# Optimization experiments

Hardware: AMD Instinct MI355X
Metric: run time of the kernel (lower is better)

Reference implementation:

```python
import jax, jax.numpy as jnp
from jax import lax
import numpy as np

B = 2; Hs = 48; Ws = 48
DIM = 768; NH = 6; NP = 4; DH = DIM // NH; HID = int(DIM * 0.25)
LIN = Hs * Ws                    # feat tokens (single deform level)
LQ = 21 * (Hs * Ws) // 4         # query tokens: (2H*2W)+(H*W)+(H/2*W/2)


def _ln(x, g, b, eps=1e-6):
    m = jnp.mean(x, -1, keepdims=True)
    v = jnp.mean((x - m) ** 2, -1, keepdims=True)
    return (x - m) * lax.rsqrt(v + eps) * g + b


def _bilinear_sample(value, loc, Hf, Wf):
    """value: [B,NH,Hf*Wf,DH]; loc: [B,Lq,NH,NP,2] normalized to [0,1].
    Matches F.grid_sample(align_corners=False, padding_mode='zeros')."""
    Bq, nH = value.shape[0], value.shape[1]
    Lq = loc.shape[1]
    x = loc[..., 0] * Wf - 0.5
    y = loc[..., 1] * Hf - 0.5
    x0 = jnp.floor(x); y0 = jnp.floor(y)
    wx1 = x - x0; wy1 = y - y0
    x0i = x0.astype(jnp.int32); y0i = y0.astype(jnp.int32)

    def tr(a):  # [B,Lq,NH,NP] -> [B,NH,Lq*NP]
        return jnp.transpose(a, (0, 2, 1, 3)).reshape(Bq, nH, Lq * NP)

    def gather(yi, xi):
        valid = ((xi >= 0) & (xi < Wf) & (yi >= 0) & (yi < Hf)).astype(value.dtype)
        idx = jnp.clip(yi, 0, Hf - 1) * Wf + jnp.clip(xi, 0, Wf - 1)
        g = jnp.take_along_axis(value, tr(idx)[..., None], axis=2)  # [B,NH,Lq*NP,DH]
        return g * tr(valid)[..., None]

    out = (gather(y0i, x0i) * tr((1 - wy1) * (1 - wx1))[..., None]
         + gather(y0i, x0i + 1) * tr((1 - wy1) * wx1)[..., None]
         + gather(y0i + 1, x0i) * tr(wy1 * (1 - wx1))[..., None]
         + gather(y0i + 1, x0i + 1) * tr(wy1 * wx1)[..., None])
    return out.reshape(Bq, nH, Lq, NP, DH)


def _dwconv(x_tokens, w, b, h, w_):
    Bq, n_tok, C = x_tokens.shape
    img = jnp.transpose(x_tokens, (0, 2, 1)).reshape(Bq, C, h, w_)
    y = lax.conv_general_dilated(img, w, (1, 1), 'SAME',
                                 dimension_numbers=('NCHW', 'OIHW', 'NCHW'),
                                 feature_group_count=C) + b[None, :, None, None]
    return jnp.transpose(y.reshape(Bq, C, h * w_), (0, 2, 1))


def _forward(query, reference_points, feat, qn_g, qn_b, fn_g, fn_b, vW, vb,
             soW, sob, awW, awb, opW, opb, mn_g, mn_b,
             fc1W, fc1b, dwW, dwb, fc2W, fc2b, H, W):
    Bq, Lq, C = query.shape
    q = _ln(query, qn_g, qn_b)
    v = _ln(feat, fn_g, fn_b) @ vW + vb                             # [B,Lin,C]
    value = jnp.transpose(v.reshape(Bq, -1, NH, DH), (0, 2, 1, 3))  # [B,NH,Lin,DH]
    offs = (q @ soW + sob).reshape(Bq, Lq, NH, NP, 2)
    attw = jax.nn.softmax((q @ awW + awb).reshape(Bq, Lq, NH, NP), axis=-1)
    norm = jnp.asarray([W, H], dtype=q.dtype)                       # (x,y) normalizer
    loc = reference_points.reshape(Bq, Lq, 1, 1, 2) + offs / norm   # [B,Lq,NH,NP,2]
    samp = _bilinear_sample(value, loc, H, W)                       # [B,NH,Lq,NP,DH]
    aw = jnp.transpose(attw, (0, 2, 1, 3))[..., None]               # [B,NH,Lq,NP,1]
    out = jnp.sum(samp * aw, axis=3)                                # [B,NH,Lq,DH]
    out = jnp.transpose(out, (0, 2, 1, 3)).reshape(Bq, Lq, C) @ opW + opb
    x = query + out                                                 # residual
    # multi-scale conv MLP
    h = _ln(x, mn_g, mn_b) @ fc1W + fc1b                            # [B,Lq,HID]
    n = Lq // 21
    h = jnp.concatenate([
        _dwconv(h[:, :16 * n], dwW, dwb, 2 * H, 2 * W),
        _dwconv(h[:, 16 * n:20 * n], dwW, dwb, H, W),
        _dwconv(h[:, 20 * n:], dwW, dwb, H // 2, W // 2)], axis=1)
    h = jax.nn.gelu(h, approximate=False)
    h = h @ fc2W + fc2b
    return x + h


def setup_inputs():
    key = jax.random.key(0)
    ks = jax.random.split(key, 16)
    s = 0.02
    return dict(
        query=jax.random.normal(ks[0], (B, LQ, DIM), jnp.float32),
        reference_points=jax.random.uniform(ks[1], (B, LQ, 1, 2), jnp.float32),
        feat=jax.random.normal(ks[2], (B, LIN, DIM), jnp.float32),
        spatial_shapes=jnp.array([[Hs, Ws]], jnp.int32),
        level_start_index=jnp.array([0], jnp.int32),
        H=Hs, W=Ws,
        qn_g=jnp.ones((DIM,)), qn_b=jnp.zeros((DIM,)),
        fn_g=jnp.ones((DIM,)), fn_b=jnp.zeros((DIM,)),
        mn_g=jnp.ones((DIM,)), mn_b=jnp.zeros((DIM,)),
        vW=s * jax.random.normal(ks[3], (DIM, DIM)), vb=jnp.zeros((DIM,)),
        soW=s * jax.random.normal(ks[4], (DIM, NH * NP * 2)),
        sob=0.5 * jax.random.normal(ks[5], (NH * NP * 2,)),
        awW=s * jax.random.normal(ks[6], (DIM, NH * NP)), awb=jnp.zeros((NH * NP,)),
        opW=s * jax.random.normal(ks[7], (DIM, DIM)), opb=jnp.zeros((DIM,)),
        fc1W=s * jax.random.normal(ks[8], (DIM, HID)), fc1b=jnp.zeros((HID,)),
        dwW=s * jax.random.normal(ks[9], (HID, 1, 3, 3)), dwb=jnp.zeros((HID,)),
        fc2W=s * jax.random.normal(ks[10], (HID, DIM)), fc2b=jnp.zeros((DIM,)),
    )


def reference(query, reference_points, feat, spatial_shapes, level_start_index, H, W,
              qn_g, qn_b, fn_g, fn_b, mn_g, mn_b, vW, vb, soW, sob, awW, awb,
              opW, opb, fc1W, fc1b, dwW, dwb, fc2W, fc2b):
    del spatial_shapes, level_start_index  # single level; H,W are static ints
    return _forward(query, reference_points, feat, qn_g, qn_b, fn_g, fn_b, vW, vb,
                    soW, sob, awW, awb, opW, opb, mn_g, mn_b,
                    fc1W, fc1b, dwW, dwb, fc2W, fc2b, H, W)
```

## Files before the change

### kernel.cpp

```cpp
#include <hip/hip_runtime.h>

#define NB    2
#define LQT   12096
#define LINT  2304
#define DIMC  768
#define NHD   6
#define NPT   4
#define DHD   128
#define HIDC  192
#define HH    48
#define WW    48

typedef __attribute__((ext_vector_type(8))) short bf16x8;
typedef __attribute__((ext_vector_type(4))) float f32x4;
typedef __attribute__((ext_vector_type(8))) unsigned short u16x8;

__device__ __forceinline__ unsigned short f2bf(float f) {
  unsigned int u = __builtin_bit_cast(unsigned int, f);
  u += 0x7FFFu + ((u >> 16) & 1u);
  return (unsigned short)(u >> 16);
}

__device__ __forceinline__ void gload16(const unsigned short* g, unsigned short* l) {
  __builtin_amdgcn_global_load_lds(
      (const __attribute__((address_space(1))) unsigned int*)g,
      (__attribute__((address_space(3))) unsigned int*)l, 16, 0, 0);
}

__global__ __launch_bounds__(256) void pack_wt(const float* __restrict__ src,
                                               unsigned short* __restrict__ dst,
                                               int K, int N, int rows) {
  size_t i = (size_t)blockIdx.x * 256 + threadIdx.x;
  if (i >= (size_t)rows * K) return;
  int n = (int)(i / K), k = (int)(i % K);
  float v = (n < N) ? src[(size_t)k * N + n] : 0.f;
  dst[i] = f2bf(v);
}

__global__ __launch_bounds__(256) void pack_soaw(const float* __restrict__ soW,
                                                 const float* __restrict__ awW,
                                                 const float* __restrict__ sob,
                                                 const float* __restrict__ awb,
                                                 unsigned short* __restrict__ dst,
                                                 float* __restrict__ bdst) {
  size_t i = (size_t)blockIdx.x * 256 + threadIdx.x;
  if (i < 128) bdst[i] = (i < 48) ? sob[i] : (i < 72 ? awb[i - 48] : 0.f);
  if (i >= (size_t)128 * DIMC) return;
  int n = (int)(i / DIMC), k = (int)(i % DIMC);
  float v = (n < 48) ? soW[(size_t)k * 48 + n]
                     : (n < 72 ? awW[(size_t)k * 24 + (n - 48)] : 0.f);
  dst[i] = f2bf(v);
}

__global__ __launch_bounds__(256) void ln_to_bf16(const float* __restrict__ in,
                                                  const float* __restrict__ gamma,
                                                  const float* __restrict__ beta,
                                                  unsigned short* __restrict__ out) {
  const int row = blockIdx.x;
  const int t = threadIdx.x;
  const float* x = in + (size_t)row * DIMC;
  float v0 = x[t], v1 = x[t + 256], v2 = x[t + 512];
  float s = v0 + v1 + v2;
  float s2 = v0 * v0 + v1 * v1 + v2 * v2;
#pragma unroll
  for (int o = 32; o > 0; o >>= 1) {
    s += __shfl_down(s, o);
    s2 += __shfl_down(s2, o);
  }
  __shared__ float red[8];
  const int wave = t >> 6, lane = t & 63;
  if (lane == 0) { red[wave] = s; red[wave + 4] = s2; }
  __syncthreads();
  float S = red[0] + red[1] + red[2] + red[3];
  float S2 = red[4] + red[5] + red[6] + red[7];
  float mean = S * (1.0f / DIMC);
  float var = S2 * (1.0f / DIMC) - mean * mean;
  float inv = rsqrtf(var + 1e-6f);
  unsigned short* o0 = out + (size_t)row * DIMC;
  o0[t]       = f2bf((v0 - mean) * inv * gamma[t]       + beta[t]);
  o0[t + 256] = f2bf((v1 - mean) * inv * gamma[t + 256] + beta[t + 256]);
  o0[t + 512] = f2bf((v2 - mean) * inv * gamma[t + 512] + beta[t + 512]);
}

template <bool HAS_ADD>
__global__ __launch_bounds__(256) void gemm_bt(const unsigned short* __restrict__ A,
                                               const unsigned short* __restrict__ Bt,
                                               const float* __restrict__ bias,
                                               const float* __restrict__ add,
                                               float* __restrict__ out,
                                               int M, int N, int K, int nn) {
  __shared__ unsigned short As[3][128 * 32];
  __shared__ unsigned short Bs[3][128 * 32];
  const int t = threadIdx.x;
  const int wave = t >> 6, lane = t & 63;

  const int nwg = gridDim.x;
  const int qq = nwg >> 3, rr = nwg & 7;
  const int xcd = blockIdx.x & 7, pos = blockIdx.x >> 3;
  const int swz = ((xcd < rr) ? xcd * (qq + 1) : rr * (qq + 1) + (xcd - rr) * qq) + pos;
  const int m0 = (swz / nn) * 128;
  const int n0 = (swz % nn) * 128;

  const int wm = (wave >> 1) * 64, wn = (wave & 1) * 64;
  const int lr = lane & 15;
  const int lg = lane >> 4;

  const int srow = wave * 16 + (lane >> 2);
  const int sslot = lane & 3;

  auto stage = [&](int buf, int k0) {
#pragma unroll
    for (int i = 0; i < 2; ++i) {
      const int row = srow + i * 64;
      const int ca = sslot ^ ((row >> 1) & 3);
      gload16(A  + (size_t)(m0 + row) * K + k0 + ca * 8, &As[buf][(wave * 16 + i * 64) * 32]);
      gload16(Bt + (size_t)(n0 + row) * K + k0 + ca * 8, &Bs[buf][(wave * 16 + i * 64) * 32]);
    }
  };

  f32x4 acc[4][4] = {};
  const int NT = K >> 5;

  stage(0, 0);
  if (NT > 1) stage(1, 32);
  if (NT > 2) stage(2, 64);

  int buf = 0;
  for (int kt = 0; kt < NT; ++kt) {
    if (kt < NT - 2)       asm volatile("s_waitcnt vmcnt(8)" ::: "memory");
    else if (kt == NT - 2) asm volatile("s_waitcnt vmcnt(4)" ::: "memory");
    else                   asm volatile("s_waitcnt vmcnt(0)" ::: "memory");
    __builtin_amdgcn_s_barrier();
    __builtin_amdgcn_sched_barrier(0);

    bf16x8 af[4], bg[4];
#pragma unroll
    for (int i = 0; i < 4; ++i) {
      int row = wm + i * 16 + lr;
      int slot = lg ^ ((row >> 1) & 3);
      af[i] = *(const bf16x8*)(&As[buf][row * 32 + slot * 8]);
      row = wn + i * 16 + lr;
      slot = lg ^ ((row >> 1) & 3);
      bg[i] = *(const bf16x8*)(&Bs[buf][row * 32 + slot * 8]);
    }
    asm volatile("s_waitcnt lgkmcnt(0)" ::: "memory");
    __builtin_amdgcn_sched_barrier(0);
    __builtin_amdgcn_s_barrier();

    if (kt + 3 < NT) stage(buf, (kt + 3) * 32);

#pragma unroll
    for (int i = 0; i < 4; ++i)
#pragma unroll
      for (int j = 0; j < 4; ++j)
        acc[i][j] = __builtin_amdgcn_mfma_f32_16x16x32_bf16(af[i], bg[j], acc[i][j], 0, 0, 0);

    buf = (buf == 2) ? 0 : buf + 1;
  }

  const int orow = lg * 4;
#pragma unroll
  for (int i = 0; i < 4; ++i) {
#pragma unroll
    for (int j = 0; j < 4; ++j) {
      const int n = n0 + wn + j * 16 + lr;
      if (n < N) {
#pragma unroll
        for (int r = 0; r < 4; ++r) {
          const int m = m0 + wm + i * 16 + orow + r;
          float v = acc[i][j][r] + bias[n];
          if (HAS_ADD) v += add[(size_t)m * N + n];
          out[(size_t)m * N + n] = v;
        }
      }
    }
  }
}

__global__ __launch_bounds__(192) void deform_attn(const float* __restrict__ soaw,
                                                   const float* __restrict__ rp,
                                                   const float* __restrict__ value,
                                                   unsigned short* __restrict__ attn) {
  const int row = blockIdx.x;
  const int b = row / LQT;
  const int t = threadIdx.x;
  const int h = t >> 5;
  const int l = t & 31;
  const float* sa = soaw + (size_t)row * 128;
  const float bx = rp[(size_t)row * 2 + 0] * (float)WW - 0.5f;
  const float by = rp[(size_t)row * 2 + 1] * (float)HH - 0.5f;

  float lg0 = sa[48 + h * 4 + 0], lg1 = sa[48 + h * 4 + 1];
  float lg2 = sa[48 + h * 4 + 2], lg3 = sa[48 + h * 4 + 3];
  float mx = fmaxf(fmaxf(lg0, lg1), fmaxf(lg2, lg3));
  float e0 = expf(lg0 - mx), e1 = expf(lg1 - mx), e2 = expf(lg2 - mx), e3 = expf(lg3 - mx);
  float inv = 1.0f / (e0 + e1 + e2 + e3);
  float awp[4] = {e0 * inv, e1 * inv, e2 * inv, e3 * inv};

  const float* vb = value + (size_t)b * LINT * DIMC + h * DHD + l * 4;
  float ax = 0.f, ay = 0.f, az = 0.f, aw = 0.f;
#pragma unroll
  for (int p = 0; p < 4; ++p) {
    float fx = bx + sa[h * 8 + p * 2 + 0];
    float fy = by + sa[h * 8 + p * 2 + 1];
    float x0f = floorf(fx), y0f = floorf(fy);
    float wx = fx - x0f, wy = fy - y0f;
    int x0 = (int)x0f, y0 = (int)y0f;
#pragma unroll
    for (int dy = 0; dy < 2; ++dy) {
#pragma unroll
      for (int dx = 0; dx < 2; ++dx) {
        int xi = x0 + dx, yi = y0 + dy;
        float w = (dy ? wy : 1.f - wy) * (dx ? wx : 1.f - wx) * awp[p];
        if (xi < 0 || xi >= WW || yi < 0 || yi >= HH) w = 0.f;
        int xc = min(max(xi, 0), WW - 1), yc = min(max(yi, 0), HH - 1);
        const float4 g = *(const float4*)(vb + (size_t)(yc * WW + xc) * DIMC);
        ax += w * g.x; ay += w * g.y; az += w * g.z; aw += w * g.w;
      }
    }
  }
  unsigned short* op = attn + (size_t)row * DIMC + h * DHD + l * 4;
  ushort4 ov;
  ov.x = f2bf(ax); ov.y = f2bf(ay); ov.z = f2bf(az); ov.w = f2bf(aw);
  *(ushort4*)op = ov;
}

__global__ __launch_bounds__(192) void dwconv_gelu(const float* __restrict__ h1,
                                                   const float* __restrict__ dwW,
                                                   const float* __restrict__ dwb,
                                                   unsigned short* __restrict__ out) {
  const int blk = blockIdx.x;
  const int b = blk / LQT;
  const int q = blk % LQT;
  int base, Wi, Hi;
  if (q < 9216)       { base = 0;     Wi = 96; Hi = 96; }
  else if (q < 11520) { base = 9216;  Wi = 48; Hi = 48; }
  else                { base = 11520; Wi = 24; Hi = 24; }
  const int loc = q - base;
  const int y = loc / Wi, x = loc % Wi;
  const int c = threadIdx.x;
  const float* src = h1 + ((size_t)b * LQT + base) * HIDC + c;
  float acc = dwb[c];
#pragma unroll
  for (int dy = -1; dy <= 1; ++dy) {
    int yy = y + dy;
    if (yy < 0 || yy >= Hi) continue;
#pragma unroll
    for (int dx = -1; dx <= 1; ++dx) {
      int xx = x + dx;
      if (xx < 0 || xx >= Wi) continue;
      acc += dwW[c * 9 + (dy + 1) * 3 + (dx + 1)] * src[(size_t)(yy * Wi + xx) * HIDC];
    }
  }
  float g = 0.5f * acc * (1.0f + erff(acc * 0.70710678118654752f));
  out[(size_t)blk * HIDC + c] = f2bf(g);
}

extern "C" void kernel_launch(void* const* d_in, const int* in_sizes, int n_in,
                              void* d_out, int out_size, void* d_ws, size_t ws_size,
                              hipStream_t stream) {
  const float* query = (const float*)d_in[0];
  const float* rp    = (const float*)d_in[1];
  const float* feat  = (const float*)d_in[2];
  const float* qn_g  = (const float*)d_in[7];
  const float* qn_b  = (const float*)d_in[8];
  const float* fn_g  = (const float*)d_in[9];
  const float* fn_b  = (const float*)d_in[10];
  const float* mn_g  = (const float*)d_in[11];
  const float* mn_b  = (const float*)d_in[12];
  const float* vW    = (const float*)d_in[13];
  const float* vb    = (const float*)d_in[14];
  const float* soW   = (const float*)d_in[15];
  const float* sob   = (const float*)d_in[16];
  const float* awW   = (const float*)d_in[17];
  const float* awb   = (const float*)d_in[18];
  const float* opW   = (const float*)d_in[19];
  const float* opb   = (const float*)d_in[20];
  const float* fc1W  = (const float*)d_in[21];
  const float* fc1b  = (const float*)d_in[22];
  const float* dwW   = (const float*)d_in[23];
  const float* dwb   = (const float*)d_in[24];
  const float* fc2W  = (const float*)d_in[25];
  const float* fc2b  = (const float*)d_in[26];
  float* out = (float*)d_out;
  (void)in_sizes; (void)n_in; (void)out_size; (void)ws_size;

  char* ws = (char*)d_ws;
  size_t off = 0;
  auto alloc = [&](size_t bytes) -> void* {
    off = (off + 255) & ~(size_t)255;
    void* p = ws + off;
    off += bytes;
    return p;
  };

  const int MQ = NB * LQT;
  const int MF = NB * LINT;

  unsigned short* vWt    = (unsigned short*)alloc((size_t)768 * 768 * 2);
  unsigned short* opWt   = (unsigned short*)alloc((size_t)768 * 768 * 2);
  unsigned short* soawWt = (unsigned short*)alloc((size_t)128 * 768 * 2);
  unsigned short* fc1Wt  = (unsigned short*)alloc((size_t)256 * 768 * 2);
  unsigned short* fc2Wt  = (unsigned short*)alloc((size_t)768 * 192 * 2);
  float*          soawb  = (float*)alloc(128 * 4);
  unsigned short* f_ln   = (unsigned short*)alloc((size_t)MF * DIMC * 2);
  unsigned short* q_ln   = (unsigned short*)alloc((size_t)MQ * DIMC * 2);
  float*          value  = (float*)alloc((size_t)MF * DIMC * 4);
  float*          soaw   = (float*)alloc((size_t)MQ * 128 * 4);
  unsigned short* attnb  = (unsigned short*)alloc((size_t)MQ * DIMC * 2);
  float*          xbuf   = (float*)alloc((size_t)MQ * DIMC * 4);

  float* h1 = (float*)attnb;
  unsigned short* coutb = (unsigned short*)soaw;
  unsigned short* lnx = q_ln;

  pack_wt<<<dim3((768 * 768 + 255) / 256), dim3(256), 0, stream>>>(vW, vWt, 768, 768, 768);
  pack_wt<<<dim3((768 * 768 + 255) / 256), dim3(256), 0, stream>>>(opW, opWt, 768, 768, 768);
  pack_wt<<<dim3((256 * 768 + 255) / 256), dim3(256), 0, stream>>>(fc1W, fc1Wt, 768, 192, 256);
  pack_wt<<<dim3((768 * 192 + 255) / 256), dim3(256), 0, stream>>>(fc2W, fc2Wt, 192, 768, 768);
  pack_soaw<<<dim3((128 * 768 + 255) / 256), dim3(256), 0, stream>>>(soW, awW, sob, awb, soawWt, soawb);

  ln_to_bf16<<<dim3(MF), dim3(256), 0, stream>>>(feat, fn_g, fn_b, f_ln);
  ln_to_bf16<<<dim3(MQ), dim3(256), 0, stream>>>(query, qn_g, qn_b, q_ln);

  gemm_bt<false><<<dim3((MF / 128) * 6), dim3(256), 0, stream>>>(f_ln, vWt, vb, nullptr, value, MF, 768, 768, 6);

  gemm_bt<false><<<dim3(MQ / 128), dim3(256), 0, stream>>>(q_ln, soawWt, soawb, nullptr, soaw, MQ, 128, 768, 1);

  deform_attn<<<dim3(MQ), dim3(192), 0, stream>>>(soaw, rp, value, attnb);

  gemm_bt<true><<<dim3((MQ / 128) * 6), dim3(256), 0, stream>>>(attnb, opWt, opb, query, xbuf, MQ, 768, 768, 6);

  ln_to_bf16<<<dim3(MQ), dim3(256), 0, stream>>>(xbuf, mn_g, mn_b, lnx);

  gemm_bt<false><<<dim3((MQ / 128) * 2), dim3(256), 0, stream>>>(lnx, fc1Wt, fc1b, nullptr, h1, MQ, 192, 768, 2);

  dwconv_gelu<<<dim3(MQ), dim3(192), 0, stream>>>(h1, dwW, dwb, coutb);

  gemm_bt<true><<<dim3((MQ / 128) * 6), dim3(256), 0, stream>>>(coutb, fc2Wt, fc2b, xbuf, out, MQ, 768, 192, 6);
}
```

Before: 337.3 us.

## Templatize GEMM tile shapes per layer and store residual intermediate in bf16

The GEMM kernel is now templated on per-wave tile counts, so each layer gets its own block shape. The value and soaw GEMMs use 64x128 tiles, the out-proj uses 256x128 tiles over a padded M, and fc1 uses 128x64 tiles so the padded fc1 weight is no longer needed. The residual buffer xbuf is stored as bf16 and the following LN and fc2 read it as bf16, which halves that traffic. The cost is lower residual precision and reliance on padded attn rows, which are only partly written.

```diff
diff --git a/kernel.cpp b/kernel.cpp
--- a/kernel.cpp
+++ b/kernel.cpp
@@ -13,18 +13,30 @@
 
 typedef __attribute__((ext_vector_type(8))) short bf16x8;
 typedef __attribute__((ext_vector_type(4))) float f32x4;
-typedef __attribute__((ext_vector_type(8))) unsigned short u16x8;
 
 __device__ __forceinline__ unsigned short f2bf(float f) {
   unsigned int u = __builtin_bit_cast(unsigned int, f);
   u += 0x7FFFu + ((u >> 16) & 1u);
   return (unsigned short)(u >> 16);
 }
+__device__ __forceinline__ float bf2f(unsigned short h) {
+  unsigned int u = ((unsigned int)h) << 16;
+  return __builtin_bit_cast(float, u);
+}
 
 __device__ __forceinline__ void gload16(const unsigned short* g, unsigned short* l) {
   __builtin_amdgcn_global_load_lds(
       (const __attribute__((address_space(1))) unsigned int*)g,
       (__attribute__((address_space(3))) unsigned int*)l, 16, 0, 0);
+}
+
+template <int N> __device__ __forceinline__ void wait_vm() {
+  if constexpr (N == 0)       asm volatile("s_waitcnt vmcnt(0)" ::: "memory");
+  else if constexpr (N == 3)  asm volatile("s_waitcnt vmcnt(3)" ::: "memory");
+  else if constexpr (N == 4)  asm volatile("s_waitcnt vmcnt(4)" ::: "memory");
+  else if constexpr (N == 6)  asm volatile("s_waitcnt vmcnt(6)" ::: "memory");
+  else if constexpr (N == 8)  asm volatile("s_waitcnt vmcnt(8)" ::: "memory");
+  else if constexpr (N == 12) asm volatile("s_waitcnt vmcnt(12)" ::: "memory");
 }
 
 __global__ __launch_bounds__(256) void pack_wt(const float* __restrict__ src,
@@ -52,14 +64,21 @@
   dst[i] = f2bf(v);
 }
 
-__global__ __launch_bounds__(256) void ln_to_bf16(const float* __restrict__ in,
+template <bool IN_BF16>
+__global__ __launch_bounds__(256) void ln_to_bf16(const void* __restrict__ in_,
                                                   const float* __restrict__ gamma,
                                                   const float* __restrict__ beta,
                                                   unsigned short* __restrict__ out) {
   const int row = blockIdx.x;
   const int t = threadIdx.x;
-  const float* x = in + (size_t)row * DIMC;
-  float v0 = x[t], v1 = x[t + 256], v2 = x[t + 512];
+  float v0, v1, v2;
+  if (IN_BF16) {
+    const unsigned short* x = (const unsigned short*)in_ + (size_t)row * DIMC;
+    v0 = bf2f(x[t]); v1 = bf2f(x[t + 256]); v2 = bf2f(x[t + 512]);
+  } else {
+    const float* x = (const float*)in_ + (size_t)row * DIMC;
+    v0 = x[t]; v1 = x[t + 256]; v2 = x[t + 512];
+  }
   float s = v0 + v1 + v2;
   float s2 = v0 * v0 + v1 * v1 + v2 * v2;
 #pragma unroll
@@ -82,15 +101,19 @@
   o0[t + 512] = f2bf((v2 - mean) * inv * gamma[t + 512] + beta[t + 512]);
 }
 
-template <bool HAS_ADD>
+template <int WM, int WN, bool HAS_ADD, bool ADD_BF16, bool OUT_BF16>
 __global__ __launch_bounds__(256) void gemm_bt(const unsigned short* __restrict__ A,
                                                const unsigned short* __restrict__ Bt,
                                                const float* __restrict__ bias,
-                                               const float* __restrict__ add,
-                                               float* __restrict__ out,
+                                               const void* __restrict__ add_,
+                                               void* __restrict__ out_,
                                                int M, int N, int K, int nn) {
-  __shared__ unsigned short As[3][128 * 32];
-  __shared__ unsigned short Bs[3][128 * 32];
+  constexpr int BM = 2 * WM * 16;
+  constexpr int BN = 2 * WN * 16;
+  constexpr int LPS = (BM + BN) / 64;
+  constexpr int CA = BM * 4;
+  __shared__ unsigned short As[3][BM * 32];
+  __shared__ unsigned short Bs[3][BN * 32];
   const int t = threadIdx.x;
   const int wave = t >> 6, lane = t & 63;
 
@@ -98,50 +121,56 @@
   const int qq = nwg >> 3, rr = nwg & 7;
   const int xcd = blockIdx.x & 7, pos = blockIdx.x >> 3;
   const int swz = ((xcd < rr) ? xcd * (qq + 1) : rr * (qq + 1) + (xcd - rr) * qq) + pos;
-  const int m0 = (swz / nn) * 128;
-  const int n0 = (swz % nn) * 128;
-
-  const int wm = (wave >> 1) * 64, wn = (wave & 1) * 64;
+  const int m0 = (swz / nn) * BM;
+  const int n0 = (swz % nn) * BN;
+
+  const int wm = (wave >> 1) * (WM * 16), wn = (wave & 1) * (WN * 16);
   const int lr = lane & 15;
   const int lg = lane >> 4;
 
-  const int srow = wave * 16 + (lane >> 2);
-  const int sslot = lane & 3;
-
   auto stage = [&](int buf, int k0) {
 #pragma unroll
-    for (int i = 0; i < 2; ++i) {
-      const int row = srow + i * 64;
-      const int ca = sslot ^ ((row >> 1) & 3);
-      gload16(A  + (size_t)(m0 + row) * K + k0 + ca * 8, &As[buf][(wave * 16 + i * 64) * 32]);
-      gload16(Bt + (size_t)(n0 + row) * K + k0 + ca * 8, &Bs[buf][(wave * 16 + i * 64) * 32]);
+    for (int i = 0; i < LPS; ++i) {
+      const int c = t + i * 256;
+      if (c < CA) {
+        const int row = c >> 2, slot = c & 3;
+        const int ca = slot ^ ((row >> 1) & 3);
+        gload16(A + (size_t)(m0 + row) * K + k0 + ca * 8, &As[buf][c * 8]);
+      } else {
+        const int c2 = c - CA, row = c2 >> 2, slot = c2 & 3;
+        const int ca = slot ^ ((row >> 1) & 3);
+        gload16(Bt + (size_t)(n0 + row) * K + k0 + ca * 8, &Bs[buf][c2 * 8]);
+      }
     }
   };
 
-  f32x4 acc[4][4] = {};
+  f32x4 acc[WM][WN] = {};
   const int NT = K >> 5;
 
   stage(0, 0);
-  if (NT > 1) stage(1, 32);
-  if (NT > 2) stage(2, 64);
+  stage(1, 32);
+  stage(2, 64);
 
   int buf = 0;
   for (int kt = 0; kt < NT; ++kt) {
-    if (kt < NT - 2)       asm volatile("s_waitcnt vmcnt(8)" ::: "memory");
-    else if (kt == NT - 2) asm volatile("s_waitcnt vmcnt(4)" ::: "memory");
-    else                   asm volatile("s_waitcnt vmcnt(0)" ::: "memory");
+    if (kt < NT - 2)       wait_vm<2 * LPS>();
+    else if (kt == NT - 2) wait_vm<LPS>();
+    else                   wait_vm<0>();
     __builtin_amdgcn_s_barrier();
     __builtin_amdgcn_sched_barrier(0);
 
-    bf16x8 af[4], bg[4];
-#pragma unroll
-    for (int i = 0; i < 4; ++i) {
-      int row = wm + i * 16 + lr;
-      int slot = lg ^ ((row >> 1) & 3);
+    bf16x8 af[WM], bg[WN];
+#pragma unroll
+    for (int i = 0; i < WM; ++i) {
+      const int row = wm + i * 16 + lr;
+      const int slot = lg ^ ((row >> 1) & 3);
       af[i] = *(const bf16x8*)(&As[buf][row * 32 + slot * 8]);
-      row = wn + i * 16 + lr;
-      slot = lg ^ ((row >> 1) & 3);
-      bg[i] = *(const bf16x8*)(&Bs[buf][row * 32 + slot * 8]);
+    }
+#pragma unroll
+    for (int j = 0; j < WN; ++j) {
+      const int row = wn + j * 16 + lr;
+      const int slot = lg ^ ((row >> 1) & 3);
+      bg[j] = *(const bf16x8*)(&Bs[buf][row * 32 + slot * 8]);
     }
     asm volatile("s_waitcnt lgkmcnt(0)" ::: "memory");
     __builtin_amdgcn_sched_barrier(0);
@@ -150,27 +179,34 @@
     if (kt + 3 < NT) stage(buf, (kt + 3) * 32);
 
 #pragma unroll
-    for (int i = 0; i < 4; ++i)
-#pragma unroll
-      for (int j = 0; j < 4; ++j)
+    for (int i = 0; i < WM; ++i)
+#pragma unroll
+      for (int j = 0; j < WN; ++j)
         acc[i][j] = __builtin_amdgcn_mfma_f32_16x16x32_bf16(af[i], bg[j], acc[i][j], 0, 0, 0);
 
     buf = (buf == 2) ? 0 : buf + 1;
   }
 
   const int orow = lg * 4;
-#pragma unroll
-  for (int i = 0; i < 4; ++i) {
-#pragma unroll
-    for (int j = 0; j < 4; ++j) {
+  const float* addf = (const float*)add_;
+  const unsigned short* addb = (const unsigned short*)add_;
+  float* outf = (float*)out_;
+  unsigned short* outb = (unsigned short*)out_;
+#pragma unroll
+  for (int i = 0; i < WM; ++i) {
+#pragma unroll
+    for (int j = 0; j < WN; ++j) {
       const int n = n0 + wn + j * 16 + lr;
       if (n < N) {
 #pragma unroll
         for (int r = 0; r < 4; ++r) {
           const int m = m0 + wm + i * 16 + orow + r;
-          float v = acc[i][j][r] + bias[n];
-          if (HAS_ADD) v += add[(size_t)m * N + n];
-          out[(size_t)m * N + n] = v;
+          if (m < M) {
+            float v = acc[i][j][r] + bias[n];
+            if (HAS_ADD) v += ADD_BF16 ? bf2f(addb[(size_t)m * N + n]) : addf[(size_t)m * N + n];
+            if (OUT_BF16) outb[(size_t)m * N + n] = f2bf(v);
+            else          outf[(size_t)m * N + n] = v;
+          }
         }
       }
     }
@@ -295,20 +331,21 @@
   };
 
   const int MQ = NB * LQT;
+  const int MQP = 24320;
   const int MF = NB * LINT;
 
   unsigned short* vWt    = (unsigned short*)alloc((size_t)768 * 768 * 2);
   unsigned short* opWt   = (unsigned short*)alloc((size_t)768 * 768 * 2);
   unsigned short* soawWt = (unsigned short*)alloc((size_t)128 * 768 * 2);
-  unsigned short* fc1Wt  = (unsigned short*)alloc((size_t)256 * 768 * 2);
+  unsigned short* fc1Wt  = (unsigned short*)alloc((size_t)192 * 768 * 2);
   unsigned short* fc2Wt  = (unsigned short*)alloc((size_t)768 * 192 * 2);
   float*          soawb  = (float*)alloc(128 * 4);
   unsigned short* f_ln   = (unsigned short*)alloc((size_t)MF * DIMC * 2);
   unsigned short* q_ln   = (unsigned short*)alloc((size_t)MQ * DIMC * 2);
   float*          value  = (float*)alloc((size_t)MF * DIMC * 4);
   float*          soaw   = (float*)alloc((size_t)MQ * 128 * 4);
-  unsigned short* attnb  = (unsigned short*)alloc((size_t)MQ * DIMC * 2);
-  float*          xbuf   = (float*)alloc((size_t)MQ * DIMC * 4);
+  unsigned short* attnb  = (unsigned short*)alloc((size_t)MQP * DIMC * 2);
+  unsigned short* xbuf   = (unsigned short*)alloc((size_t)MQ * DIMC * 2);
 
   float* h1 = (float*)attnb;
   unsigned short* coutb = (unsigned short*)soaw;
@@ -316,26 +353,31 @@
 
   pack_wt<<<dim3((768 * 768 + 255) / 256), dim3(256), 0, stream>>>(vW, vWt, 768, 768, 768);
   pack_wt<<<dim3((768 * 768 + 255) / 256), dim3(256), 0, stream>>>(opW, opWt, 768, 768, 768);
-  pack_wt<<<dim3((256 * 768 + 255) / 256), dim3(256), 0, stream>>>(fc1W, fc1Wt, 768, 192, 256);
+  pack_wt<<<dim3((192 * 768 + 255) / 256), dim3(256), 0, stream>>>(fc1W, fc1Wt, 768, 192, 192);
   pack_wt<<<dim3((768 * 192 + 255) / 256), dim3(256), 0, stream>>>(fc2W, fc2Wt, 192, 768, 768);
   pack_soaw<<<dim3((128 * 768 + 255) / 256), dim3(256), 0, stream>>>(soW, awW, sob, awb, soawWt, soawb);
 
-  ln_to_bf16<<<dim3(MF), dim3(256), 0, stream>>>(feat, fn_g, fn_b, f_ln);
-  ln_to_bf16<<<dim3(MQ), dim3(256), 0, stream>>>(query, qn_g, qn_b, q_ln);
-
-  gemm_bt<false><<<dim3((MF / 128) * 6), dim3(256), 0, stream>>>(f_ln, vWt, vb, nullptr, value, MF, 768, 768, 6);
-
-  gemm_bt<false><<<dim3(MQ / 128), dim3(256), 0, stream>>>(q_ln, soawWt, soawb, nullptr, soaw, MQ, 128, 768, 1);
+  ln_to_bf16<false><<<dim3(MF), dim3(256), 0, stream>>>(feat, fn_g, fn_b, f_ln);
+  ln_to_bf16<false><<<dim3(MQ), dim3(256), 0, stream>>>(query, qn_g, qn_b, q_ln);
+
+  gemm_bt<2, 4, false, false, false><<<dim3((MF / 64) * 6), dim3(256), 0, stream>>>(
+      f_ln, vWt, vb, nullptr, value, MF, 768, 768, 6);
+
+  gemm_bt<2, 4, false, false, false><<<dim3(MQ / 64), dim3(256), 0, stream>>>(
+      q_ln, soawWt, soawb, nullptr, soaw, MQ, 128, 768, 1);
 
   deform_attn<<<dim3(MQ), dim3(192), 0, stream>>>(soaw, rp, value, attnb);
 
-  gemm_bt<true><<<dim3((MQ / 128) * 6), dim3(256), 0, stream>>>(attnb, opWt, opb, query, xbuf, MQ, 768, 768, 6);
-
-  ln_to_bf16<<<dim3(MQ), dim3(256), 0, stream>>>(xbuf, mn_g, mn_b, lnx);
-
-  gemm_bt<false><<<dim3((MQ / 128) * 2), dim3(256), 0, stream>>>(lnx, fc1Wt, fc1b, nullptr, h1, MQ, 192, 768, 2);
+  gemm_bt<8, 4, true, false, true><<<dim3((MQP / 256) * 6), dim3(256), 0, stream>>>(
+      attnb, opWt, opb, query, xbuf, MQ, 768, 768, 6);
+
+  ln_to_bf16<true><<<dim3(MQ), dim3(256), 0, stream>>>(xbuf, mn_g, mn_b, lnx);
+
+  gemm_bt<4, 2, false, false, false><<<dim3((MQ / 128) * 3), dim3(256), 0, stream>>>(
+      lnx, fc1Wt, fc1b, nullptr, h1, MQ, 192, 768, 3);
 
   dwconv_gelu<<<dim3(MQ), dim3(192), 0, stream>>>(h1, dwW, dwb, coutb);
 
-  gemm_bt<true><<<dim3((MQ / 128) * 6), dim3(256), 0, stream>>>(coutb, fc2Wt, fc2b, xbuf, out, MQ, 768, 192, 6);
-}
+  gemm_bt<4, 4, true, true, false><<<dim3((MQ / 128) * 6), dim3(256), 0, stream>>>(
+      coutb, fc2Wt, fc2b, xbuf, out, MQ, 768, 192, 6);
+}
```

Measured after the change: 428.9 us. 27.2% more time.
